# Kernel optimization log

Measured on AMD Instinct MI355X. Metric: run time of the kernel, lower is better.

## Reference

```python
import jax, jax.numpy as jnp
import numpy as np

N_TF = 11
H = 1024
B = 2048


def setup_inputs() -> dict:
    key = jax.random.key(0)
    ks = jax.random.split(key, 10)
    s = 0.02  # weight init scale
    return {
        "h_stack": jax.random.normal(ks[0], (B, N_TF, H), dtype=jnp.float32),
        "base_confidence": jax.random.uniform(ks[1], (B,), dtype=jnp.float32),
        "kW1": jax.random.normal(ks[2], (H, H // 2), dtype=jnp.float32) * s,
        "kb1": jnp.zeros((H // 2,), jnp.float32),
        "kW2": jax.random.normal(ks[3], (H // 2, 1), dtype=jnp.float32) * s,
        "kb2": jnp.zeros((1,), jnp.float32),
        "lW1": jax.random.normal(ks[4], (H, H // 2), dtype=jnp.float32) * s,
        "lb1": jnp.zeros((H // 2,), jnp.float32),
        "lW2": jax.random.normal(ks[5], (H // 2, 1), dtype=jnp.float32) * s,
        "lb2": jnp.zeros((1,), jnp.float32),
        "dW1": jax.random.normal(ks[6], (2 * H, H), dtype=jnp.float32) * s,
        "db1": jnp.zeros((H,), jnp.float32),
        "dW2": jax.random.normal(ks[7], (H, 1), dtype=jnp.float32) * s,
        "db2": jnp.zeros((1,), jnp.float32),
        "kinetic_weight": jnp.asarray(1.0, jnp.float32),
        "local_weight": jnp.asarray(0.5, jnp.float32),
        "interaction_weight": jnp.asarray(0.3, jnp.float32),
        "temperature": jnp.asarray(1.0, jnp.float32),
    }


def reference(h_stack, base_confidence, kW1, kb1, kW2, kb2, lW1, lb1, lW2, lb2,
              dW1, db1, dW2, db2, kinetic_weight, local_weight,
              interaction_weight, temperature):
    n_tf = h_stack.shape[1]
    h = h_stack.shape[2]
    ii, jj = np.triu_indices(n_tf, k=1)  # 55 upper-triangular pairs
    dist_w = jnp.asarray(1.0 / (np.abs(ii - jj) + 1.0), dtype=h_stack.dtype)
    n_pairs = ii.shape[0]

    # kinetic: mean over TFs of small MLP, negated
    k_hid = jax.nn.relu(jnp.einsum('bth,hd->btd', h_stack, kW1) + kb1)
    k_per = (jnp.einsum('btd,do->bto', k_hid, kW2) + kb2)[..., 0]  # [B, T]
    kinetic_energy = -kinetic_weight * k_per.mean(axis=1)

    # local: relu of per-TF MLP, mean
    l_hid = jax.nn.relu(jnp.einsum('bth,hd->btd', h_stack, lW1) + lb1)
    l_per = (jnp.einsum('btd,do->bto', l_hid, lW2) + lb2)[..., 0]
    local_energy = local_weight * jax.nn.relu(l_per).mean(axis=1)

    # interaction: concat-MLP over all pairs, batched.
    # cat([h_i, h_j]) @ dW1 == h_i @ dW1[:H] + h_j @ dW1[H:]
    dW1a, dW1b = dW1[:h], dW1[h:]
    pre_i = jnp.einsum('bth,hd->btd', h_stack, dW1a)  # [B, T, H]
    pre_j = jnp.einsum('bth,hd->btd', h_stack, dW1b)  # [B, T, H]
    hid = jax.nn.relu(pre_i[:, ii] + pre_j[:, jj] + db1)  # [B, P, H]
    dis = jax.nn.relu((jnp.einsum('bpd,do->bpo', hid, dW2) + db2)[..., 0])  # [B, P]
    interaction_energy = interaction_weight * (dis * dist_w).sum(axis=1) / n_pairs

    total_energy = kinetic_energy + local_energy + interaction_energy
    energy_confidence = jax.nn.sigmoid(-total_energy / (jnp.abs(temperature) + 0.1))
    adjusted_confidence = base_confidence * energy_confidence
    return jnp.stack([total_energy, kinetic_energy, local_energy,
                      interaction_energy, energy_confidence,
                      adjusted_confidence], axis=0)  # [6, B]
```

## Files before the change

kernel.cpp:

```cpp
#include <hip/hip_runtime.h>
#include <hip/hip_bf16.h>
#include <math.h>

typedef __attribute__((ext_vector_type(8))) short bf16x8;
typedef __attribute__((ext_vector_type(4))) float f32x4;

#define NBATCH   2048
#define GB       4
#define ROWS     44
#define ROWSP    48
#define LDSA_BYTES (ROWSP * 1024 * 2)
#define STG_TILE   (ROWSP * 20)
#define STG_WAVE   (2 * STG_TILE)
#define LDS_TOTAL  (LDSA_BYTES + 8 * STG_WAVE * 4)

__device__ unsigned short g_wsB2[(size_t)3072 * 1024];

static constexpr int II_[55] = {
    0,0,0,0,0,0,0,0,0,0, 1,1,1,1,1,1,1,1,1, 2,2,2,2,2,2,2,2,
    3,3,3,3,3,3,3, 4,4,4,4,4,4, 5,5,5,5,5, 6,6,6,6, 7,7,7, 8,8, 9};
static constexpr int JJ_[55] = {
    1,2,3,4,5,6,7,8,9,10, 2,3,4,5,6,7,8,9,10, 3,4,5,6,7,8,9,10,
    4,5,6,7,8,9,10, 5,6,7,8,9,10, 6,7,8,9,10, 7,8,9,10, 8,9,10, 9,10, 10};

__device__ __forceinline__ unsigned short f32_to_bf16u(float f) {
    unsigned u = __float_as_uint(f);
    u += 0x7fffu + ((u >> 16) & 1u);
    return (unsigned short)(u >> 16);
}

__global__ void pack_weights(const float* __restrict__ kW1,
                             const float* __restrict__ lW1,
                             const float* __restrict__ dW1) {
    const int t = blockIdx.x * 256 + threadIdx.x;
    const int lane = t & 63;
    const int kk   = (t >> 6) & 31;
    const int g    = t >> 11;
    const int col  = g * 16 + (lane & 15);
    const int k0   = kk * 32 + (lane >> 4) * 8;
    const float* src; int ncol, c;
    if (col < 512)       { src = kW1;                          ncol = 512;  c = col; }
    else if (col < 1024) { src = lW1;                          ncol = 512;  c = col - 512; }
    else if (col < 2048) { src = dW1;                          ncol = 1024; c = col - 1024; }
    else                 { src = dW1 + (size_t)1024 * 1024;    ncol = 1024; c = col - 2048; }
    bf16x8 v;
    #pragma unroll
    for (int j = 0; j < 8; ++j)
        v[j] = (short)f32_to_bf16u(src[(size_t)(k0 + j) * ncol + c]);
    *(bf16x8*)(g_wsB2 + (size_t)t * 8) = v;
}

__launch_bounds__(512, 2)
__global__ void energy_mfma(
    const float* __restrict__ h_stack, const float* __restrict__ base_conf,
    const float* __restrict__ kb1, const float* __restrict__ kW2,
    const float* __restrict__ kb2, const float* __restrict__ lb1,
    const float* __restrict__ lW2, const float* __restrict__ lb2,
    const float* __restrict__ db1, const float* __restrict__ dW2,
    const float* __restrict__ db2,
    const float* __restrict__ kwp, const float* __restrict__ lwp,
    const float* __restrict__ iwp, const float* __restrict__ tmpp,
    float* __restrict__ out)
{
    extern __shared__ char smem[];
    char* Ab = smem;
    float* stageBase = (float*)(smem + LDSA_BYTES);

    const int tid  = threadIdx.x;
    const int wv   = tid >> 6;
    const int ln   = tid & 63;
    const int lo16 = ln & 15;
    const int hi4  = ln >> 4;
    const unsigned xorv = (unsigned)((ln & 7) << 4);

    {
        const size_t hbase = (size_t)blockIdx.x * (ROWS * 1024);
        #pragma unroll
        for (int i = 0; i < 11; ++i) {
            int idx = tid + i * 512;
            int row = idx >> 7;
            int kc  = idx & 127;
            const float* src = h_stack + hbase + (size_t)row * 1024 + kc * 8;
            float4 a = *(const float4*)src;
            float4 b = *(const float4*)(src + 4);
            bf16x8 v;
            v[0] = (short)f32_to_bf16u(a.x); v[1] = (short)f32_to_bf16u(a.y);
            v[2] = (short)f32_to_bf16u(a.z); v[3] = (short)f32_to_bf16u(a.w);
            v[4] = (short)f32_to_bf16u(b.x); v[5] = (short)f32_to_bf16u(b.y);
            v[6] = (short)f32_to_bf16u(b.z); v[7] = (short)f32_to_bf16u(b.w);
            unsigned kbyte = ((unsigned)(kc * 16)) ^ ((unsigned)((row & 7) << 4));
            *(bf16x8*)(Ab + row * 2048 + kbyte) = v;
        }
        {
            int row = ROWS + (tid >> 7);
            int kc  = tid & 127;
            unsigned kbyte = ((unsigned)(kc * 16)) ^ ((unsigned)((row & 7) << 4));
            bf16x8 z = {0,0,0,0,0,0,0,0};
            *(bf16x8*)(Ab + row * 2048 + kbyte) = z;
        }
    }
    __syncthreads();

    float kin_part = 0.f, loc_part = 0.f;
    float accP[55];
    #pragma unroll
    for (int p = 0; p < 55; ++p) accP[p] = 0.f;

    float* stg0 = stageBase + wv * STG_WAVE;
    float* stg1 = stg0 + STG_TILE;

    auto readA = [&](int m, int kk) -> bf16x8 {
        unsigned addr = (unsigned)((16 * m + lo16) * 2048)
                      + ((unsigned)(kk * 64 + hi4 * 16) ^ xorv);
        return *(const bf16x8*)(Ab + addr);
    };

    #pragma unroll 1
    for (int ui = 0; ui < 6; ++ui) {
        const int u = wv + ui * 8;
        int g0, g1, g2, g3;
        if (u < 16) { g0 = 4 * u; g1 = 4 * u + 1; g2 = 4 * u + 2; g3 = 4 * u + 3; }
        else        { int v = u - 16;
                      g0 = 64 + 2 * v; g1 = 128 + 2 * v;
                      g2 = 65 + 2 * v; g3 = 129 + 2 * v; }

        const unsigned short* bp0 = g_wsB2 + (size_t)g0 * 16384 + ln * 8;
        const unsigned short* bp1 = g_wsB2 + (size_t)g1 * 16384 + ln * 8;
        const unsigned short* bp2 = g_wsB2 + (size_t)g2 * 16384 + ln * 8;
        const unsigned short* bp3 = g_wsB2 + (size_t)g3 * 16384 + ln * 8;

        f32x4 acc[4][3];
        #pragma unroll
        for (int q = 0; q < 4; ++q)
            #pragma unroll
            for (int m = 0; m < 3; ++m) acc[q][m] = (f32x4){0.f, 0.f, 0.f, 0.f};

        auto ldB = [&](const unsigned short* p, int kk) -> bf16x8 {
            return *(const bf16x8*)(p + (size_t)kk * 512);
        };
        auto mfma12 = [&](bf16x8 a0, bf16x8 a1, bf16x8 a2,
                          bf16x8 b0, bf16x8 b1, bf16x8 b2, bf16x8 b3) {
            acc[0][0] = __builtin_amdgcn_mfma_f32_16x16x32_bf16(a0, b0, acc[0][0], 0, 0, 0);
            acc[0][1] = __builtin_amdgcn_mfma_f32_16x16x32_bf16(a1, b0, acc[0][1], 0, 0, 0);
            acc[0][2] = __builtin_amdgcn_mfma_f32_16x16x32_bf16(a2, b0, acc[0][2], 0, 0, 0);
            acc[1][0] = __builtin_amdgcn_mfma_f32_16x16x32_bf16(a0, b1, acc[1][0], 0, 0, 0);
            acc[1][1] = __builtin_amdgcn_mfma_f32_16x16x32_bf16(a1, b1, acc[1][1], 0, 0, 0);
            acc[1][2] = __builtin_amdgcn_mfma_f32_16x16x32_bf16(a2, b1, acc[1][2], 0, 0, 0);
            acc[2][0] = __builtin_amdgcn_mfma_f32_16x16x32_bf16(a0, b2, acc[2][0], 0, 0, 0);
            acc[2][1] = __builtin_amdgcn_mfma_f32_16x16x32_bf16(a1, b2, acc[2][1], 0, 0, 0);
            acc[2][2] = __builtin_amdgcn_mfma_f32_16x16x32_bf16(a2, b2, acc[2][2], 0, 0, 0);
            acc[3][0] = __builtin_amdgcn_mfma_f32_16x16x32_bf16(a0, b3, acc[3][0], 0, 0, 0);
            acc[3][1] = __builtin_amdgcn_mfma_f32_16x16x32_bf16(a1, b3, acc[3][1], 0, 0, 0);
            acc[3][2] = __builtin_amdgcn_mfma_f32_16x16x32_bf16(a2, b3, acc[3][2], 0, 0, 0);
        };

        bf16x8 A0 = readA(0, 0), A1 = readA(1, 0), A2 = readA(2, 0);
        bf16x8 B0 = ldB(bp0, 0), B1 = ldB(bp1, 0), B2 = ldB(bp2, 0), B3 = ldB(bp3, 0);
        bf16x8 C0 = ldB(bp0, 1), C1 = ldB(bp1, 1), C2 = ldB(bp2, 1), C3 = ldB(bp3, 1);

        #pragma unroll 2
        for (int kk = 0; kk < 31; ++kk) {
            bf16x8 a0 = A0, a1 = A1, a2 = A2;
            A0 = readA(0, kk + 1); A1 = readA(1, kk + 1); A2 = readA(2, kk + 1);
            bf16x8 b0 = B0, b1 = B1, b2 = B2, b3 = B3;
            B0 = C0; B1 = C1; B2 = C2; B3 = C3;
            if (kk < 30) {
                C0 = ldB(bp0, kk + 2); C1 = ldB(bp1, kk + 2);
                C2 = ldB(bp2, kk + 2); C3 = ldB(bp3, kk + 2);
            }
            mfma12(a0, a1, a2, b0, b1, b2, b3);
        }
        mfma12(A0, A1, A2, B0, B1, B2, B3);

        if (u < 16) {
            const float* b1arr = (u < 8) ? kb1 : lb1;
            const float* w2arr = (u < 8) ? kW2 : lW2;
            const int colrel0 = (u < 8) ? u * 64 : (u - 8) * 64;
            float part = 0.f;
            #pragma unroll
            for (int q = 0; q < 4; ++q) {
                const int colrel = colrel0 + q * 16 + lo16;
                const float b1v = b1arr[colrel];
                const float w2v = w2arr[colrel];
                float* sb = (q & 1) ? stg1 : stg0;
                #pragma unroll
                for (int m = 0; m < 3; ++m)
                    #pragma unroll
                    for (int r = 0; r < 4; ++r) {
                        const int row = 16 * m + 4 * hi4 + r;
                        sb[row * 20 + lo16] = fmaxf(acc[q][m][r] + b1v, 0.f) * w2v;
                    }
                asm volatile("s_waitcnt lgkmcnt(0)" ::: "memory");
                if (ln < ROWS) {
                    const f32x4* rp = (const f32x4*)(sb + ln * 20);
                    float s = 0.f;
                    #pragma unroll
                    for (int c4 = 0; c4 < 4; ++c4) {
                        f32x4 vv = rp[c4];
                        s += vv[0] + vv[1] + vv[2] + vv[3];
                    }
                    part += s;
                }
            }
            if (u < 8) kin_part += part; else loc_part += part;
        } else {
            const int v = u - 16;
            #pragma unroll
            for (int half = 0; half < 2; ++half) {
                const int dcol = (2 * v + half) * 16 + lo16;
                const float db1v = db1[dcol];
                const float dw2v = dW2[dcol];
                #pragma unroll
                for (int m = 0; m < 3; ++m)
                    #pragma unroll
                    for (int r = 0; r < 4; ++r) {
                        const int row = 16 * m + 4 * hi4 + r;
                        stg0[row * 20 + lo16] = acc[2 * half + 0][m][r];
                        stg1[row * 20 + lo16] = acc[2 * half + 1][m][r];
                    }
                asm volatile("s_waitcnt lgkmcnt(0)" ::: "memory");
                float pi[11], pj[11];
                #pragma unroll
                for (int t = 0; t < 11; ++t) {
                    const int row = 11 * hi4 + t;
                    pi[t] = stg0[row * 20 + lo16] + db1v;
                    pj[t] = stg1[row * 20 + lo16];
                }
                asm volatile("s_waitcnt lgkmcnt(0)" ::: "memory");
                #pragma unroll
                for (int p = 0; p < 55; ++p) {
                    const float s = pi[II_[p]] + pj[JJ_[p]];
                    accP[p] = fmaf(fmaxf(s, 0.f), dw2v, accP[p]);
                }
            }
        }
    }

    __syncthreads();
    float* kinbuf  = stageBase;
    float* locbuf  = stageBase + 512;
    float* pairbuf = stageBase + 1024;
    float* pairres = stageBase + 2816;
    float* kinrow  = stageBase + 3040;
    float* locrow  = stageBase + 3104;

    kinbuf[wv * 64 + ln] = kin_part;
    locbuf[wv * 64 + ln] = loc_part;
    #pragma unroll
    for (int p = 0; p < 55; ++p) {
        float vsum = accP[p];
        vsum += __shfl_xor(vsum, 1);
        vsum += __shfl_xor(vsum, 2);
        vsum += __shfl_xor(vsum, 4);
        vsum += __shfl_xor(vsum, 8);
        if (lo16 == 0) pairbuf[wv * 224 + hi4 * 56 + p] = vsum;
    }
    __syncthreads();

    if (tid < 220) {
        const int b = tid / 55, p = tid % 55;
        float s = db2[0];
        #pragma unroll
        for (int w = 0; w < 8; ++w) s += pairbuf[w * 224 + b * 56 + p];
        s = fmaxf(s, 0.f);
        const float dw = 1.0f / (float)(JJ_[p] - II_[p] + 1);
        pairres[b * 56 + p] = s * dw;
    }
    if (tid >= 256 && tid < 304) {
        const int r = tid - 256;
        float sk = 0.f, sl = 0.f;
        #pragma unroll
        for (int w = 0; w < 8; ++w) { sk += kinbuf[w * 64 + r]; sl += locbuf[w * 64 + r]; }
        kinrow[r] = sk; locrow[r] = sl;
    }
    __syncthreads();

    if (tid < 4) {
        const int b = tid;
        const float kw = kwp[0], lw = lwp[0], iw = iwp[0], temp = tmpp[0];
        float ks = 0.f;
        #pragma unroll
        for (int t = 0; t < 11; ++t) ks += kinrow[11 * b + t];
        const float kinetic = -kw * (ks * (1.f / 11.f) + kb2[0]);
        float ls = 0.f;
        #pragma unroll
        for (int t = 0; t < 11; ++t) ls += fmaxf(locrow[11 * b + t] + lb2[0], 0.f);
        const float local_e = lw * (ls * (1.f / 11.f));
        float is = 0.f;
        #pragma unroll
        for (int p = 0; p < 55; ++p) is += pairres[b * 56 + p];
        const float inter = iw * (is * (1.f / 55.f));
        const float total = kinetic + local_e + inter;
        const float ec = 1.f / (1.f + expf(total / (fabsf(temp) + 0.1f)));
        const int gb = blockIdx.x * 4 + b;
        out[0 * NBATCH + gb] = total;
        out[1 * NBATCH + gb] = kinetic;
        out[2 * NBATCH + gb] = local_e;
        out[3 * NBATCH + gb] = inter;
        out[4 * NBATCH + gb] = ec;
        out[5 * NBATCH + gb] = base_conf[gb] * ec;
    }
}

extern "C" void kernel_launch(void* const* d_in, const int* in_sizes, int n_in,
                              void* d_out, int out_size, void* d_ws, size_t ws_size,
                              hipStream_t stream) {
    const float* h_stack   = (const float*)d_in[0];
    const float* base_conf = (const float*)d_in[1];
    const float* kW1 = (const float*)d_in[2];
    const float* kb1 = (const float*)d_in[3];
    const float* kW2 = (const float*)d_in[4];
    const float* kb2 = (const float*)d_in[5];
    const float* lW1 = (const float*)d_in[6];
    const float* lb1 = (const float*)d_in[7];
    const float* lW2 = (const float*)d_in[8];
    const float* lb2 = (const float*)d_in[9];
    const float* dW1 = (const float*)d_in[10];
    const float* db1 = (const float*)d_in[11];
    const float* dW2 = (const float*)d_in[12];
    const float* db2 = (const float*)d_in[13];
    const float* kwp = (const float*)d_in[14];
    const float* lwp = (const float*)d_in[15];
    const float* iwp = (const float*)d_in[16];
    const float* tmpp= (const float*)d_in[17];
    float* out = (float*)d_out;

    hipLaunchKernelGGL(pack_weights, dim3(1536), dim3(256), 0, stream, kW1, lW1, dW1);

    hipFuncSetAttribute((const void*)energy_mfma,
                        hipFuncAttributeMaxDynamicSharedMemorySize, LDS_TOTAL);
    hipLaunchKernelGGL(energy_mfma, dim3(512), dim3(512), LDS_TOTAL, stream,
                       h_stack, base_conf, kb1, kW2, kb2, lb1, lW2, lb2,
                       db1, dW2, db2, kwp, lwp, iwp, tmpp, out);
}
```

Baseline: 262.1 us.

## Split output columns across two blocks per row group and add finalize kernel

Each group of four batch rows is now handled by two blocks, each covering half of the weight column groups. That doubles the grid from 512 to 1024 blocks, which should fill the GPU's compute units better. Per-block partial pair sums and kinetic/local partials go to a global workspace, and a new small finalize kernel combines them, applies the biases and ReLU, and writes the outputs. In exchange, each block still loads and converts its full activation tile, so h_stack is read twice, and there is an extra kernel launch plus global round-trip traffic.

New measurement: 289.2 us. 1.1x slower.

```diff
diff --git a/kernel.cpp b/kernel.cpp
--- a/kernel.cpp
+++ b/kernel.cpp
@@ -15,6 +15,8 @@
 #define LDS_TOTAL  (LDSA_BYTES + 8 * STG_WAVE * 4)
 
 __device__ unsigned short g_wsB2[(size_t)3072 * 1024];
+
+__device__ float g_ws2[(size_t)NBATCH * 128];
 
 static constexpr int II_[55] = {
     0,0,0,0,0,0,0,0,0,0, 1,1,1,1,1,1,1,1,1, 2,2,2,2,2,2,2,2,
@@ -52,15 +54,10 @@
 
 __launch_bounds__(512, 2)
 __global__ void energy_mfma(
-    const float* __restrict__ h_stack, const float* __restrict__ base_conf,
+    const float* __restrict__ h_stack,
     const float* __restrict__ kb1, const float* __restrict__ kW2,
-    const float* __restrict__ kb2, const float* __restrict__ lb1,
-    const float* __restrict__ lW2, const float* __restrict__ lb2,
-    const float* __restrict__ db1, const float* __restrict__ dW2,
-    const float* __restrict__ db2,
-    const float* __restrict__ kwp, const float* __restrict__ lwp,
-    const float* __restrict__ iwp, const float* __restrict__ tmpp,
-    float* __restrict__ out)
+    const float* __restrict__ lb1, const float* __restrict__ lW2,
+    const float* __restrict__ db1, const float* __restrict__ dW2)
 {
     extern __shared__ char smem[];
     char* Ab = smem;
@@ -73,8 +70,13 @@
     const int hi4  = ln >> 4;
     const unsigned xorv = (unsigned)((ln & 7) << 4);
 
+    const int bx = blockIdx.x;
+    const int x  = bx & 7;
+    const int colHalf  = x & 1;
+    const int rowBlock = (bx >> 3) * 4 + (x >> 1);
+
     {
-        const size_t hbase = (size_t)blockIdx.x * (ROWS * 1024);
+        const size_t hbase = (size_t)rowBlock * (ROWS * 1024);
         #pragma unroll
         for (int i = 0; i < 11; ++i) {
             int idx = tid + i * 512;
@@ -116,8 +118,8 @@
     };
 
     #pragma unroll 1
-    for (int ui = 0; ui < 6; ++ui) {
-        const int u = wv + ui * 8;
+    for (int ui = 0; ui < 3; ++ui) {
+        const int u = 24 * colHalf + ui * 8 + wv;
         int g0, g1, g2, g3;
         if (u < 16) { g0 = 4 * u; g1 = 4 * u + 1; g2 = 4 * u + 2; g3 = 4 * u + 3; }
         else        { int v = u - 16;
@@ -240,7 +242,6 @@
     float* kinbuf  = stageBase;
     float* locbuf  = stageBase + 512;
     float* pairbuf = stageBase + 1024;
-    float* pairres = stageBase + 2816;
     float* kinrow  = stageBase + 3040;
     float* locrow  = stageBase + 3104;
 
@@ -259,47 +260,72 @@
 
     if (tid < 220) {
         const int b = tid / 55, p = tid % 55;
-        float s = db2[0];
+        float s = 0.f;
         #pragma unroll
         for (int w = 0; w < 8; ++w) s += pairbuf[w * 224 + b * 56 + p];
+        const int gb = rowBlock * 4 + b;
+        g_ws2[(size_t)gb * 128 + (colHalf ? 67 : 12) + p] = s;
+    }
+    if (colHalf == 0) {
+        if (tid >= 256 && tid < 304) {
+            const int r = tid - 256;
+            float sk = 0.f, sl = 0.f;
+            #pragma unroll
+            for (int w = 0; w < 8; ++w) { sk += kinbuf[w * 64 + r]; sl += locbuf[w * 64 + r]; }
+            kinrow[r] = sk; locrow[r] = sl;
+        }
+        __syncthreads();
+        if (tid < 4) {
+            const int b = tid;
+            const int gb = rowBlock * 4 + b;
+            float ks = 0.f;
+            #pragma unroll
+            for (int t = 0; t < 11; ++t) ks += kinrow[11 * b + t];
+            g_ws2[(size_t)gb * 128 + 0] = ks;
+            #pragma unroll
+            for (int t = 0; t < 11; ++t)
+                g_ws2[(size_t)gb * 128 + 1 + t] = locrow[11 * b + t];
+        }
+    }
+}
+
+__global__ void finalize(
+    const float* __restrict__ base_conf,
+    const float* __restrict__ kb2, const float* __restrict__ lb2,
+    const float* __restrict__ db2,
+    const float* __restrict__ kwp, const float* __restrict__ lwp,
+    const float* __restrict__ iwp, const float* __restrict__ tmpp,
+    float* __restrict__ out)
+{
+    const int gb = blockIdx.x * 256 + threadIdx.x;
+    if (gb >= NBATCH) return;
+    const float* w = g_ws2 + (size_t)gb * 128;
+    const float kw = kwp[0], lw = lwp[0], iw = iwp[0], temp = tmpp[0];
+
+    const float kinetic = -kw * (w[0] * (1.f / 11.f) + kb2[0]);
+
+    float ls = 0.f;
+    #pragma unroll
+    for (int t = 0; t < 11; ++t) ls += fmaxf(w[1 + t] + lb2[0], 0.f);
+    const float local_e = lw * (ls * (1.f / 11.f));
+
+    float is = 0.f;
+    #pragma unroll
+    for (int p = 0; p < 55; ++p) {
+        float s = w[12 + p] + w[67 + p] + db2[0];
         s = fmaxf(s, 0.f);
-        const float dw = 1.0f / (float)(JJ_[p] - II_[p] + 1);
-        pairres[b * 56 + p] = s * dw;
-    }
-    if (tid >= 256 && tid < 304) {
-        const int r = tid - 256;
-        float sk = 0.f, sl = 0.f;
-        #pragma unroll
-        for (int w = 0; w < 8; ++w) { sk += kinbuf[w * 64 + r]; sl += locbuf[w * 64 + r]; }
-        kinrow[r] = sk; locrow[r] = sl;
-    }
-    __syncthreads();
-
-    if (tid < 4) {
-        const int b = tid;
-        const float kw = kwp[0], lw = lwp[0], iw = iwp[0], temp = tmpp[0];
-        float ks = 0.f;
-        #pragma unroll
-        for (int t = 0; t < 11; ++t) ks += kinrow[11 * b + t];
-        const float kinetic = -kw * (ks * (1.f / 11.f) + kb2[0]);
-        float ls = 0.f;
-        #pragma unroll
-        for (int t = 0; t < 11; ++t) ls += fmaxf(locrow[11 * b + t] + lb2[0], 0.f);
-        const float local_e = lw * (ls * (1.f / 11.f));
-        float is = 0.f;
-        #pragma unroll
-        for (int p = 0; p < 55; ++p) is += pairres[b * 56 + p];
-        const float inter = iw * (is * (1.f / 55.f));
-        const float total = kinetic + local_e + inter;
-        const float ec = 1.f / (1.f + expf(total / (fabsf(temp) + 0.1f)));
-        const int gb = blockIdx.x * 4 + b;
-        out[0 * NBATCH + gb] = total;
-        out[1 * NBATCH + gb] = kinetic;
-        out[2 * NBATCH + gb] = local_e;
-        out[3 * NBATCH + gb] = inter;
-        out[4 * NBATCH + gb] = ec;
-        out[5 * NBATCH + gb] = base_conf[gb] * ec;
-    }
+        is += s * (1.f / (float)(JJ_[p] - II_[p] + 1));
+    }
+    const float inter = iw * (is * (1.f / 55.f));
+
+    const float total = kinetic + local_e + inter;
+    const float ec = 1.f / (1.f + expf(total / (fabsf(temp) + 0.1f)));
+    out[0 * NBATCH + gb] = total;
+    out[1 * NBATCH + gb] = kinetic;
+    out[2 * NBATCH + gb] = local_e;
+    out[3 * NBATCH + gb] = inter;
+    out[4 * NBATCH + gb] = ec;
+    out[5 * NBATCH + gb] = base_conf[gb] * ec;
 }
 
 extern "C" void kernel_launch(void* const* d_in, const int* in_sizes, int n_in,
@@ -329,7 +355,9 @@
 
     hipFuncSetAttribute((const void*)energy_mfma,
                         hipFuncAttributeMaxDynamicSharedMemorySize, LDS_TOTAL);
-    hipLaunchKernelGGL(energy_mfma, dim3(512), dim3(512), LDS_TOTAL, stream,
-                       h_stack, base_conf, kb1, kW2, kb2, lb1, lW2, lb2,
-                       db1, dW2, db2, kwp, lwp, iwp, tmpp, out);
-}
+    hipLaunchKernelGGL(energy_mfma, dim3(1024), dim3(512), LDS_TOTAL, stream,
+                       h_stack, kb1, kW2, lb1, lW2, db1, dW2);
+
+    hipLaunchKernelGGL(finalize, dim3(8), dim3(256), 0, stream,
+                       base_conf, kb2, lb2, db2, kwp, lwp, iwp, tmpp, out);
+}
```
